# Kernel optimization log

Hardware: AMD Instinct MI355X
Metric: run time of the kernel (lower is better)

The kernel has to match this reference:

```python
import jax, jax.numpy as jnp
import numpy as np

B, K, V, N, M, TOPK = 256, 256, 256, 4000, 4000, 8
EPS = 1e-8  # torch F.cosine_similarity default eps


def setup_inputs() -> dict:
    key = jax.random.key(0)
    ks = jax.random.split(key, 6)
    query_key = jax.random.normal(ks[0], (B, K), dtype=jnp.float32)
    W_k = jax.random.normal(ks[1], (K, K), dtype=jnp.float32) / np.sqrt(K).astype(np.float32)
    b_k = jnp.zeros((K,), dtype=jnp.float32)
    assoc_matrix = jax.random.normal(ks[2], (N, K, V), dtype=jnp.float32) * 0.02
    usage_counter = jax.random.uniform(ks[3], (N,), dtype=jnp.float32) * 10.0
    memory_index = jax.random.randint(ks[4], (M,), 0, N)
    return {
        "query_key": query_key,
        "W_k": W_k,
        "b_k": b_k,
        "assoc_matrix": assoc_matrix,
        "usage_counter": usage_counter,
        "memory_index": memory_index,
        "top_k": TOPK,
    }


def reference(query_key, W_k, b_k, assoc_matrix, usage_counter, memory_index, top_k):
    # key_encoder: Linear + Tanh
    e = jnp.tanh(query_key @ W_k.T + b_k)                      # [B, K]
    # stored keys = first value-column of each used slot (irregular gather)
    stored_keys = assoc_matrix[memory_index, :, 0]             # [M, K]
    # cosine similarity (vectorized form of the per-slot python loop)
    qn = e / jnp.maximum(jnp.linalg.norm(e, axis=-1, keepdims=True), EPS)
    kn = stored_keys / jnp.maximum(jnp.linalg.norm(stored_keys, axis=-1, keepdims=True), EPS)
    sims = qn @ kn.T                                           # [B, M]
    top_sims, top_idx = jax.lax.top_k(sims, top_k)             # [B, k]
    actual = memory_index[top_idx]                             # [B, k] slot ids
    # confidence = sim * (1 + log(1 + usage))
    confidences = top_sims * (1.0 + jnp.log1p(usage_counter[actual]))
    # gather stored associations and retrieve values: e @ A[actual]
    gathered = assoc_matrix[actual]                            # [B, k, K, V]
    retrieved_values = jnp.einsum('bd,bkdv->bkv', e, gathered) # [B, k, V]
    return retrieved_values, confidences, top_sims
```

## Files before the change

### kernel.cpp

```cpp
#include <hip/hip_runtime.h>
#include <math.h>

#define BB 256
#define KK 256
#define VV 256
#define MM 4000
#define TOPK 8

__global__ void k_proj(const float* __restrict__ qk, const float* __restrict__ Wk,
                       const float* __restrict__ bk, double* __restrict__ e64,
                       double* __restrict__ qn64) {
    int b = blockIdx.x, j = threadIdx.x;
    __shared__ float q[KK];
    __shared__ double red[256];
    q[j] = qk[b * KK + j];
    __syncthreads();
    const float* w = Wk + (size_t)j * KK;
    double acc = 0.0;
#pragma unroll 4
    for (int d = 0; d < KK; ++d) acc += (double)q[d] * (double)w[d];
    double val = tanh(acc + (double)bk[j]);
    e64[b * KK + j] = val;
    red[j] = val * val;
    __syncthreads();
    for (int s = 128; s > 0; s >>= 1) {
        if (j < s) red[j] += red[j + s];
        __syncthreads();
    }
    double nrm = fmax(sqrt(red[0]), 1e-8);
    qn64[b * KK + j] = val / nrm;
}

__global__ void k_kn(const float* __restrict__ A, const int* __restrict__ midx,
                     double* __restrict__ kn64) {
    int m = blockIdx.x, t = threadIdx.x;
    size_t n = (size_t)midx[m];
    double val = (double)A[n * (size_t)(KK * VV) + (size_t)t * VV];
    __shared__ double red[256];
    red[t] = val * val;
    __syncthreads();
    for (int s = 128; s > 0; s >>= 1) {
        if (t < s) red[t] += red[t + s];
        __syncthreads();
    }
    double nrm = fmax(sqrt(red[0]), 1e-8);
    kn64[(size_t)m * KK + t] = val / nrm;
}

__global__ void __launch_bounds__(256) k_sims(
        const double* __restrict__ qn, const double* __restrict__ kn,
        double* __restrict__ sims) {
    int tx = threadIdx.x, ty = threadIdx.y;
    int tid = ty * 16 + tx;
    int m0 = blockIdx.x * 32, b0 = blockIdx.y * 32;
    __shared__ double qs[32][33], ks[32][33];
    double a00 = 0.0, a01 = 0.0, a10 = 0.0, a11 = 0.0;
    for (int kk = 0; kk < KK; kk += 32) {
#pragma unroll
        for (int i = 0; i < 4; ++i) {
            int idx = tid + i * 256;
            int r = idx >> 5, c = idx & 31;
            qs[r][c] = qn[(size_t)(b0 + r) * KK + kk + c];
            ks[r][c] = kn[(size_t)(m0 + r) * KK + kk + c];
        }
        __syncthreads();
#pragma unroll
        for (int i = 0; i < 32; ++i) {
            double q0 = qs[ty][i], q1 = qs[ty + 16][i];
            double k0 = ks[tx][i], k1 = ks[tx + 16][i];
            a00 += q0 * k0; a01 += q0 * k1;
            a10 += q1 * k0; a11 += q1 * k1;
        }
        __syncthreads();
    }
    sims[(size_t)(b0 + ty) * MM + m0 + tx]           = a00;
    sims[(size_t)(b0 + ty) * MM + m0 + tx + 16]      = a01;
    sims[(size_t)(b0 + ty + 16) * MM + m0 + tx]      = a10;
    sims[(size_t)(b0 + ty + 16) * MM + m0 + tx + 16] = a11;
}

__global__ void k_topk(const double* __restrict__ sims, const int* __restrict__ midx,
                       const float* __restrict__ usage, float* __restrict__ out_conf,
                       float* __restrict__ out_sims, int* __restrict__ acts) {
    int b = blockIdx.x, t = threadIdx.x;
    double v[TOPK];
    int id[TOPK];
#pragma unroll
    for (int i = 0; i < TOPK; ++i) { v[i] = -INFINITY; id[i] = 0x7fffffff; }
    const double* row = sims + (size_t)b * MM;
    for (int m = t; m < MM; m += 256) {
        double x = row[m];
        if (x > v[TOPK - 1]) {
            v[TOPK - 1] = x; id[TOPK - 1] = m;
#pragma unroll
            for (int i = TOPK - 1; i > 0; --i) {
                if (v[i] > v[i - 1]) {
                    double tv = v[i]; v[i] = v[i - 1]; v[i - 1] = tv;
                    int ti = id[i]; id[i] = id[i - 1]; id[i - 1] = ti;
                }
            }
        }
    }
    __shared__ double sv[256 * TOPK];
    __shared__ int si[256 * TOPK];
#pragma unroll
    for (int i = 0; i < TOPK; ++i) { sv[t * TOPK + i] = v[i]; si[t * TOPK + i] = id[i]; }
    __syncthreads();
    for (int stride = 128; stride > 0; stride >>= 1) {
        if (t < stride) {
            double* av = &sv[t * TOPK];
            int*    ai = &si[t * TOPK];
            double* bv = &sv[(t + stride) * TOPK];
            int*    bi = &si[(t + stride) * TOPK];
            double mv[TOPK]; int mi[TOPK];
            int pa = 0, pb = 0;
#pragma unroll
            for (int i = 0; i < TOPK; ++i) {
                double va = av[pa], vb = bv[pb];
                bool takeA = (va > vb) || (va == vb && ai[pa] < bi[pb]);
                if (takeA) { mv[i] = va; mi[i] = ai[pa]; ++pa; }
                else       { mv[i] = vb; mi[i] = bi[pb]; ++pb; }
            }
#pragma unroll
            for (int i = 0; i < TOPK; ++i) { av[i] = mv[i]; ai[i] = mi[i]; }
        }
        __syncthreads();
    }
    if (t < TOPK) {
        double val = sv[t];
        int idx = si[t];
        int actual = midx[idx];
        out_sims[b * TOPK + t] = (float)val;
        out_conf[b * TOPK + t] = (float)(val * (1.0 + log1p((double)usage[actual])));
        acts[b * TOPK + t] = actual;
    }
}

__global__ void __launch_bounds__(256) k_retr(
        const float* __restrict__ A, const double* __restrict__ e64,
        const int* __restrict__ acts, float* __restrict__ out) {
    int bk_ = blockIdx.x;
    int b = bk_ >> 3;
    int tid = threadIdx.x;
    int w = tid >> 6, l = tid & 63;
    size_t n = (size_t)acts[bk_];
    const float* Ap = A + n * (size_t)(KK * VV);
    __shared__ float es[KK];
    __shared__ float part[4][64][4];
    es[tid] = (float)e64[b * KK + tid];
    __syncthreads();
    float ax = 0.f, ay = 0.f, az = 0.f, aw = 0.f;
    const float* base = Ap + (size_t)(w * 64) * VV + 4 * l;
#pragma unroll 8
    for (int dd = 0; dd < 64; ++dd) {
        float ev = es[w * 64 + dd];
        const float4 a = *reinterpret_cast<const float4*>(base + (size_t)dd * VV);
        ax = fmaf(ev, a.x, ax); ay = fmaf(ev, a.y, ay);
        az = fmaf(ev, a.z, az); aw = fmaf(ev, a.w, aw);
    }
    part[w][l][0] = ax; part[w][l][1] = ay; part[w][l][2] = az; part[w][l][3] = aw;
    __syncthreads();
    int l2 = tid >> 2, j = tid & 3;
    float s = part[0][l2][j] + part[1][l2][j] + part[2][l2][j] + part[3][l2][j];
    out[(size_t)bk_ * VV + tid] = s;
}

extern "C" void kernel_launch(void* const* d_in, const int* in_sizes, int n_in,
                              void* d_out, int out_size, void* d_ws, size_t ws_size,
                              hipStream_t stream) {
    const float* qk    = (const float*)d_in[0];
    const float* Wk    = (const float*)d_in[1];
    const float* bk    = (const float*)d_in[2];
    const float* A     = (const float*)d_in[3];
    const float* usage = (const float*)d_in[4];
    const int*   midx  = (const int*)d_in[5];

    float* out   = (float*)d_out;
    float* retr  = out;
    float* conf  = out + (size_t)BB * TOPK * VV;
    float* tsims = conf + BB * TOPK;

    double* ws64  = (double*)d_ws;
    double* e64   = ws64;
    double* qn64  = e64 + BB * KK;
    double* kn64  = qn64 + BB * KK;
    double* sims  = kn64 + (size_t)MM * KK;
    int*    acts  = (int*)(sims + (size_t)BB * MM);

    k_proj<<<BB, 256, 0, stream>>>(qk, Wk, bk, e64, qn64);
    k_kn<<<MM, 256, 0, stream>>>(A, midx, kn64);
    dim3 g3(MM / 32, BB / 32), b3(16, 16);
    k_sims<<<g3, b3, 0, stream>>>(qn64, kn64, sims);
    k_topk<<<BB, 256, 0, stream>>>(sims, midx, usage, conf, tsims, acts);
    k_retr<<<BB * TOPK, 256, 0, stream>>>(A, e64, acts, retr);
}
```

Measured before the change: 175.3 us.

## Merge projection and key-norm kernels; sort retrieval blocks by slot for cache reuse

The projection and stored-key normalization kernels are fused into a single launch, with block index selecting the role, which removes one kernel launch. A new single-block bitonic sort orders the (slot, batch*k) pairs by slot id so that retrieval blocks reading the same 256 KB association matrix are scheduled next to each other and can hit in L2/MALL instead of refetching from HBM. The cost is an extra serial kernel that sorts 2048 keys in shared memory with many barriers, and the retrieval output order now depends on the unpacked index.

Result: slower. 259.7 us (+48.2%).

```diff
diff --git a/kernel.cpp b/kernel.cpp
--- a/kernel.cpp
+++ b/kernel.cpp
@@ -7,44 +7,44 @@
 #define MM 4000
 #define TOPK 8
 
-__global__ void k_proj(const float* __restrict__ qk, const float* __restrict__ Wk,
-                       const float* __restrict__ bk, double* __restrict__ e64,
-                       double* __restrict__ qn64) {
-    int b = blockIdx.x, j = threadIdx.x;
+__global__ void __launch_bounds__(256) k_prep(
+        const float* __restrict__ qk, const float* __restrict__ Wk,
+        const float* __restrict__ bk, const float* __restrict__ A,
+        const int* __restrict__ midx, double* __restrict__ e64,
+        double* __restrict__ qn64, double* __restrict__ kn64) {
+    __shared__ double red[256];
     __shared__ float q[KK];
-    __shared__ double red[256];
-    q[j] = qk[b * KK + j];
-    __syncthreads();
-    const float* w = Wk + (size_t)j * KK;
-    double acc = 0.0;
+    if (blockIdx.x < MM) {
+        int m = blockIdx.x, t = threadIdx.x;
+        size_t n = (size_t)midx[m];
+        double val = (double)A[n * (size_t)(KK * VV) + (size_t)t * VV];
+        red[t] = val * val;
+        __syncthreads();
+        for (int s = 128; s > 0; s >>= 1) {
+            if (t < s) red[t] += red[t + s];
+            __syncthreads();
+        }
+        double nrm = fmax(sqrt(red[0]), 1e-8);
+        kn64[(size_t)m * KK + t] = val / nrm;
+    } else {
+        int b = blockIdx.x - MM, j = threadIdx.x;
+        q[j] = qk[b * KK + j];
+        __syncthreads();
+        const float* w = Wk + (size_t)j * KK;
+        double acc = 0.0;
 #pragma unroll 4
-    for (int d = 0; d < KK; ++d) acc += (double)q[d] * (double)w[d];
-    double val = tanh(acc + (double)bk[j]);
-    e64[b * KK + j] = val;
-    red[j] = val * val;
-    __syncthreads();
-    for (int s = 128; s > 0; s >>= 1) {
-        if (j < s) red[j] += red[j + s];
-        __syncthreads();
-    }
-    double nrm = fmax(sqrt(red[0]), 1e-8);
-    qn64[b * KK + j] = val / nrm;
-}
-
-__global__ void k_kn(const float* __restrict__ A, const int* __restrict__ midx,
-                     double* __restrict__ kn64) {
-    int m = blockIdx.x, t = threadIdx.x;
-    size_t n = (size_t)midx[m];
-    double val = (double)A[n * (size_t)(KK * VV) + (size_t)t * VV];
-    __shared__ double red[256];
-    red[t] = val * val;
-    __syncthreads();
-    for (int s = 128; s > 0; s >>= 1) {
-        if (t < s) red[t] += red[t + s];
-        __syncthreads();
-    }
-    double nrm = fmax(sqrt(red[0]), 1e-8);
-    kn64[(size_t)m * KK + t] = val / nrm;
+        for (int d = 0; d < KK; ++d) acc += (double)q[d] * (double)w[d];
+        double val = tanh(acc + (double)bk[j]);
+        e64[b * KK + j] = val;
+        red[j] = val * val;
+        __syncthreads();
+        for (int s = 128; s > 0; s >>= 1) {
+            if (j < s) red[j] += red[j + s];
+            __syncthreads();
+        }
+        double nrm = fmax(sqrt(red[0]), 1e-8);
+        qn64[b * KK + j] = val / nrm;
+    }
 }
 
 __global__ void __launch_bounds__(256) k_sims(
@@ -136,14 +136,39 @@
     }
 }
 
+__global__ void __launch_bounds__(256) k_sort(const int* __restrict__ acts,
+                                              unsigned* __restrict__ sorted) {
+    __shared__ unsigned key[BB * TOPK];
+    int t = threadIdx.x;
+    for (int i = t; i < BB * TOPK; i += 256)
+        key[i] = ((unsigned)acts[i] << 11) | (unsigned)i;
+    __syncthreads();
+    for (int k = 2; k <= BB * TOPK; k <<= 1) {
+        for (int j = k >> 1; j > 0; j >>= 1) {
+            for (int i = t; i < BB * TOPK; i += 256) {
+                int l = i ^ j;
+                if (l > i) {
+                    bool asc = ((i & k) == 0);
+                    unsigned a = key[i], b2 = key[l];
+                    bool sw = asc ? (a > b2) : (a < b2);
+                    if (sw) { key[i] = b2; key[l] = a; }
+                }
+            }
+            __syncthreads();
+        }
+    }
+    for (int i = t; i < BB * TOPK; i += 256) sorted[i] = key[i];
+}
+
 __global__ void __launch_bounds__(256) k_retr(
         const float* __restrict__ A, const double* __restrict__ e64,
-        const int* __restrict__ acts, float* __restrict__ out) {
-    int bk_ = blockIdx.x;
+        const unsigned* __restrict__ sorted, float* __restrict__ out) {
+    unsigned keyv = sorted[blockIdx.x];
+    int bk_ = (int)(keyv & 0x7FFu);
+    size_t n = (size_t)(keyv >> 11);
     int b = bk_ >> 3;
     int tid = threadIdx.x;
     int w = tid >> 6, l = tid & 63;
-    size_t n = (size_t)acts[bk_];
     const float* Ap = A + n * (size_t)(KK * VV);
     __shared__ float es[KK];
     __shared__ float part[4][64][4];
@@ -180,17 +205,18 @@
     float* conf  = out + (size_t)BB * TOPK * VV;
     float* tsims = conf + BB * TOPK;
 
-    double* ws64  = (double*)d_ws;
-    double* e64   = ws64;
-    double* qn64  = e64 + BB * KK;
-    double* kn64  = qn64 + BB * KK;
-    double* sims  = kn64 + (size_t)MM * KK;
-    int*    acts  = (int*)(sims + (size_t)BB * MM);
-
-    k_proj<<<BB, 256, 0, stream>>>(qk, Wk, bk, e64, qn64);
-    k_kn<<<MM, 256, 0, stream>>>(A, midx, kn64);
+    double*   ws64   = (double*)d_ws;
+    double*   e64    = ws64;
+    double*   qn64   = e64 + BB * KK;
+    double*   kn64   = qn64 + BB * KK;
+    double*   sims   = kn64 + (size_t)MM * KK;
+    int*      acts   = (int*)(sims + (size_t)BB * MM);
+    unsigned* sorted = (unsigned*)(acts + BB * TOPK);
+
+    k_prep<<<MM + BB, 256, 0, stream>>>(qk, Wk, bk, A, midx, e64, qn64, kn64);
     dim3 g3(MM / 32, BB / 32), b3(16, 16);
     k_sims<<<g3, b3, 0, stream>>>(qn64, kn64, sims);
     k_topk<<<BB, 256, 0, stream>>>(sims, midx, usage, conf, tsims, acts);
-    k_retr<<<BB * TOPK, 256, 0, stream>>>(A, e64, acts, retr);
-}
+    k_sort<<<1, 256, 0, stream>>>(acts, sorted);
+    k_retr<<<BB * TOPK, 256, 0, stream>>>(A, e64, sorted, retr);
+}
```

## Retile fp64 similarity GEMM with 4x4 register blocking and transposed shared tiles

Applied to the files above, without the earlier changes.

The double-precision query-key similarity kernel moves from a 32x32 tile with 2x2 outputs per thread to a 32x64 tile computed by 128 threads, each holding a 4x4 register accumulator. Operands are stored transposed in shared memory so each thread can read them with vectorized double2 loads, cutting shared-memory traffic per FMA. Bounds checks handle the M dimension, which does not divide evenly by 64. The cost is more registers per thread and fewer threads per block, which may lower occupancy.

New measurement: 178.6 us. About the same (+1.9%).

```diff
diff --git a/kernel.cpp b/kernel.cpp
--- a/kernel.cpp
+++ b/kernel.cpp
@@ -47,36 +47,59 @@
     kn64[(size_t)m * KK + t] = val / nrm;
 }
 
-__global__ void __launch_bounds__(256) k_sims(
+#define BMS 32
+#define BNS 64
+#define KS  16
+__global__ void __launch_bounds__(128) k_sims(
         const double* __restrict__ qn, const double* __restrict__ kn,
         double* __restrict__ sims) {
-    int tx = threadIdx.x, ty = threadIdx.y;
-    int tid = ty * 16 + tx;
-    int m0 = blockIdx.x * 32, b0 = blockIdx.y * 32;
-    __shared__ double qs[32][33], ks[32][33];
-    double a00 = 0.0, a01 = 0.0, a10 = 0.0, a11 = 0.0;
-    for (int kk = 0; kk < KK; kk += 32) {
-#pragma unroll
-        for (int i = 0; i < 4; ++i) {
-            int idx = tid + i * 256;
-            int r = idx >> 5, c = idx & 31;
-            qs[r][c] = qn[(size_t)(b0 + r) * KK + kk + c];
-            ks[r][c] = kn[(size_t)(m0 + r) * KK + kk + c];
-        }
-        __syncthreads();
-#pragma unroll
-        for (int i = 0; i < 32; ++i) {
-            double q0 = qs[ty][i], q1 = qs[ty + 16][i];
-            double k0 = ks[tx][i], k1 = ks[tx + 16][i];
-            a00 += q0 * k0; a01 += q0 * k1;
-            a10 += q1 * k0; a11 += q1 * k1;
-        }
-        __syncthreads();
-    }
-    sims[(size_t)(b0 + ty) * MM + m0 + tx]           = a00;
-    sims[(size_t)(b0 + ty) * MM + m0 + tx + 16]      = a01;
-    sims[(size_t)(b0 + ty + 16) * MM + m0 + tx]      = a10;
-    sims[(size_t)(b0 + ty + 16) * MM + m0 + tx + 16] = a11;
+    __shared__ double qsT[KS][BMS + 2];
+    __shared__ double ksT[KS][BNS + 2];
+    int tid = threadIdx.x;
+    int tx = tid & 15;
+    int ty = tid >> 4;
+    int m0 = blockIdx.x * BNS;
+    int b0 = blockIdx.y * BMS;
+    double acc[4][4] = {};
+    int qr = tid >> 2;
+    int qc = (tid & 3) * 4;
+    int kr = tid >> 1;
+    int kc = (tid & 1) * 8;
+    bool kval = (m0 + kr) < MM;
+    const double* qrow = qn + (size_t)(b0 + qr) * KK;
+    const double* krow = kn + (size_t)(m0 + (kval ? kr : 0)) * KK;
+    for (int kk = 0; kk < KK; kk += KS) {
+#pragma unroll
+        for (int j = 0; j < 4; ++j)
+            qsT[qc + j][qr] = qrow[kk + qc + j];
+#pragma unroll
+        for (int j = 0; j < 8; ++j)
+            ksT[kc + j][kr] = kval ? krow[kk + kc + j] : 0.0;
+        __syncthreads();
+#pragma unroll
+        for (int i = 0; i < KS; ++i) {
+            double qv[4], kv[4];
+            *(double2*)&qv[0] = *(const double2*)&qsT[i][ty * 4];
+            *(double2*)&qv[2] = *(const double2*)&qsT[i][ty * 4 + 2];
+            *(double2*)&kv[0] = *(const double2*)&ksT[i][tx * 4];
+            *(double2*)&kv[2] = *(const double2*)&ksT[i][tx * 4 + 2];
+#pragma unroll
+            for (int a = 0; a < 4; ++a)
+#pragma unroll
+                for (int c = 0; c < 4; ++c)
+                    acc[a][c] += qv[a] * kv[c];
+        }
+        __syncthreads();
+    }
+#pragma unroll
+    for (int a = 0; a < 4; ++a) {
+        int bb = b0 + ty * 4 + a;
+#pragma unroll
+        for (int c = 0; c < 4; ++c) {
+            int mm2 = m0 + tx * 4 + c;
+            if (mm2 < MM) sims[(size_t)bb * MM + mm2] = acc[a][c];
+        }
+    }
 }
 
 __global__ void k_topk(const double* __restrict__ sims, const int* __restrict__ midx,
@@ -189,8 +212,8 @@
 
     k_proj<<<BB, 256, 0, stream>>>(qk, Wk, bk, e64, qn64);
     k_kn<<<MM, 256, 0, stream>>>(A, midx, kn64);
-    dim3 g3(MM / 32, BB / 32), b3(16, 16);
-    k_sims<<<g3, b3, 0, stream>>>(qn64, kn64, sims);
+    dim3 g3((MM + BNS - 1) / BNS, BB / BMS);
+    k_sims<<<g3, 128, 0, stream>>>(qn64, kn64, sims);
     k_topk<<<BB, 256, 0, stream>>>(sims, midx, usage, conf, tsims, acts);
     k_retr<<<BB * TOPK, 256, 0, stream>>>(A, e64, acts, retr);
 }
```
